# Performance work log

Hardware: AMD Instinct MI355X
Metric: run time of the kernel (lower is better)

## Reference

```python
import jax, jax.numpy as jnp
import numpy as np

B, S, D, H = 2, 2048, 1024, 16
HD = D // H

def setup_inputs() -> dict:
    key = jax.random.key(0)
    ks = jax.random.split(key, 9)
    s = 1.0 / np.sqrt(D)
    return {
        "x": jax.random.normal(ks[0], (B, S, D), dtype=jnp.float32),
        "Wq": jax.random.uniform(ks[1], (D, D), jnp.float32, -s, s),
        "bq": jax.random.uniform(ks[2], (D,), jnp.float32, -s, s),
        "Wk": jax.random.uniform(ks[3], (D, D), jnp.float32, -s, s),
        "bk": jax.random.uniform(ks[4], (D,), jnp.float32, -s, s),
        "Wv": jax.random.uniform(ks[5], (D, D), jnp.float32, -s, s),
        "bv": jax.random.uniform(ks[6], (D,), jnp.float32, -s, s),
        "Wo": jax.random.uniform(ks[7], (D, D), jnp.float32, -s, s),
        "bo": jax.random.uniform(ks[8], (D,), jnp.float32, -s, s),
    }

def reference(x, Wq, bq, Wk, bk, Wv, bv, Wo, bo):
    # project and split heads: [B,S,D] -> [B,H,S,HD]
    def heads(t):
        return t.reshape(B, S, H, HD).transpose(0, 2, 1, 3)
    q = heads(x @ Wq.T + bq)
    k = heads(x @ Wk.T + bk)
    v = heads(x @ Wv.T + bv)
    scores = jnp.einsum('bhqd,bhkd->bhqk', q, k) / np.sqrt(HD).astype(np.float32)
    attention_weights = jax.nn.softmax(scores, axis=-1)  # [B,H,S,S]
    out = jnp.einsum('bhqk,bhkd->bhqd', attention_weights, v)
    out = out.transpose(0, 2, 1, 3).reshape(B, S, D)
    out = out @ Wo.T + bo
    return out, attention_weights
```

## Files before the change

kernel.cpp:

```cpp
#include <hip/hip_runtime.h>
#include <stdint.h>

#define BB 2
#define SS 2048
#define DD 1024
#define HH 16
#define HDD 64

typedef _Float16 f16x8 __attribute__((ext_vector_type(8)));
typedef _Float16 f16x4 __attribute__((ext_vector_type(4)));
typedef float f32x4 __attribute__((ext_vector_type(4)));

#define MFMA16(a,b,c) __builtin_amdgcn_mfma_f32_16x16x32_f16((a),(b),(c),0,0,0)

__device__ __forceinline__ _Float16 toh(float v) { return (_Float16)v; }

__device__ __forceinline__ void gll16(const void* g, void* l) {
  __builtin_amdgcn_global_load_lds(
      (const __attribute__((address_space(1))) unsigned int*)g,
      (__attribute__((address_space(3))) unsigned int*)l, 16, 0, 0);
}

__global__ __launch_bounds__(256) void k_convert(
    const float* __restrict__ x, const float* __restrict__ Wq, const float* __restrict__ Wk,
    const float* __restrict__ Wv, const float* __restrict__ Wo, _Float16* __restrict__ ws) {
  int i = blockIdx.x * 256 + threadIdx.x;
  const float4* src; _Float16* dst; int idx;
  if (i < 1048576) { src = (const float4*)x; dst = ws; idx = i; }
  else {
    int j = i - 1048576;
    int wsel = j >> 18;
    idx = j & 262143;
    src = (const float4*)(wsel == 0 ? Wq : wsel == 1 ? Wk : wsel == 2 ? Wv : Wo);
    dst = ws + 4194304 + (size_t)wsel * 1048576;
  }
  float4 f = src[idx];
  f16x4 o = { toh(f.x), toh(f.y), toh(f.z), toh(f.w) };
  *(f16x4*)(dst + (size_t)idx * 4) = o;
}

__device__ __forceinline__ void stage2(const _Float16* g, _Float16* lds, int t) {
#pragma unroll
  for (int i = 0; i < 2; ++i) {
    const _Float16* src = g + (size_t)(i * 64 + (t >> 2)) * 1024 + (t & 3) * 8;
    gll16(src, lds + i * 2048 + t * 8);
  }
}

__device__ __forceinline__ void gemm_core(const _Float16* __restrict__ A,
                                          const _Float16* __restrict__ W,
                                          int bm, int bn, _Float16* As, _Float16* Bs,
                                          f32x4 (&acc)[4][4]) {
  const int t = threadIdx.x;
  const int l = t & 63, w = t >> 6;
  const int wr = w >> 1, wc = w & 1, li = l & 15, lg = l >> 4;
  const _Float16* Abase = A + (size_t)bm * 128 * 1024;
  const _Float16* Wbase = W + (size_t)bn * 128 * 1024;

  stage2(Abase, As, t);
  stage2(Wbase, Bs, t);
  int cur = 0;
  for (int kt = 0; kt < 32; ++kt) {
    __syncthreads();
    if (kt < 31) {
      stage2(Abase + (kt + 1) * 32, As + (cur ^ 1) * 4096, t);
      stage2(Wbase + (kt + 1) * 32, Bs + (cur ^ 1) * 4096, t);
    }
    const _Float16* Ab = As + cur * 4096;
    const _Float16* Bb = Bs + cur * 4096;
    f16x8 af[4], bfr[4];
#pragma unroll
    for (int m = 0; m < 4; ++m)
      af[m] = *(const f16x8*)(Ab + (wr * 64 + m * 16 + li) * 32 + lg * 8);
#pragma unroll
    for (int n = 0; n < 4; ++n)
      bfr[n] = *(const f16x8*)(Bb + (wc * 64 + n * 16 + li) * 32 + lg * 8);
    __builtin_amdgcn_s_setprio(1);
#pragma unroll
    for (int m = 0; m < 4; ++m)
#pragma unroll
      for (int n = 0; n < 4; ++n)
        acc[m][n] = MFMA16(af[m], bfr[n], acc[m][n]);
    __builtin_amdgcn_s_setprio(0);
    cur ^= 1;
  }
}

__global__ __launch_bounds__(256) void k_gemm_qkv(
    const _Float16* __restrict__ xb, const _Float16* __restrict__ wqb,
    const _Float16* __restrict__ wkb, const _Float16* __restrict__ wvb,
    const float* __restrict__ bq, const float* __restrict__ bk, const float* __restrict__ bv,
    _Float16* __restrict__ Qw, _Float16* __restrict__ Kw, _Float16* __restrict__ Vtw) {
  int mode = blockIdx.z;
  const _Float16* W = mode == 0 ? wqb : mode == 1 ? wkb : wvb;
  const float* bias = mode == 0 ? bq : mode == 1 ? bk : bv;
  __shared__ _Float16 As[8192], Bs[8192];
  f32x4 acc[4][4] = {};
  gemm_core(xb, W, blockIdx.y, blockIdx.x, As, Bs, acc);

  int t = threadIdx.x, l = t & 63, w = t >> 6, wr = w >> 1, wc = w & 1, li = l & 15, lg = l >> 4;
  int rb = blockIdx.y * 128 + wr * 64, cb = blockIdx.x * 128 + wc * 64;
  float scale = (mode == 0) ? 0.125f * 1.4426950408889634f : 1.0f;
#pragma unroll
  for (int n = 0; n < 4; ++n) {
    int col = cb + n * 16 + li;
    float bsv = bias[col];
    int hh = col >> 6, hd = col & 63;
#pragma unroll
    for (int m = 0; m < 4; ++m)
#pragma unroll
      for (int r = 0; r < 4; ++r) {
        int row = rb + m * 16 + lg * 4 + r;
        int bb = row >> 11, ssi = row & 2047;
        float val = (acc[m][n][r] + bsv) * scale;
        if (mode == 0)
          Qw[((size_t)(bb * HH + hh) * SS + ssi) * HDD + hd] = toh(val);
        else if (mode == 1)
          Kw[((size_t)(bb * HH + hh) * SS + ssi) * HDD + hd] = toh(val);
        else
          Vtw[((size_t)(bb * HH + hh) * HDD + hd) * SS + ssi] = toh(val);
      }
  }
}

__global__ __launch_bounds__(256) void k_flash(
    const _Float16* __restrict__ Qw, const _Float16* __restrict__ Kw,
    const _Float16* __restrict__ Vtw, float* __restrict__ mlb, _Float16* __restrict__ attnb) {
  int qb = blockIdx.x;
  int h = blockIdx.y, b = blockIdx.z;
  int t = threadIdx.x, l = t & 63, w = t >> 6;
  int li = l & 15, lg = l >> 4;
  size_t bh = (size_t)(b * HH + h);
  const _Float16* Qh = Qw + bh * SS * HDD;
  const _Float16* Kh = Kw + bh * SS * HDD;
  const _Float16* Vh = Vtw + bh * HDD * SS;
  int qrow = qb * 128 + w * 32;

  __shared__ _Float16 Kbuf[2][4096];
  __shared__ _Float16 Vbuf[2][4096];
  __shared__ _Float16 Wl[4][32][72];

  f16x8 aq[2][2];
#pragma unroll
  for (int qh = 0; qh < 2; ++qh)
#pragma unroll
    for (int s = 0; s < 2; ++s)
      aq[qh][s] = *(const f16x8*)&Qh[(size_t)(qrow + qh * 16 + li) * HDD + s * 32 + lg * 8];

  const f32x4 fzero = {0.f, 0.f, 0.f, 0.f};
  f32x4 oacc[2][4] = {{fzero, fzero, fzero, fzero}, {fzero, fzero, fzero, fzero}};
  float lsum[2][4] = {{0.f, 0.f, 0.f, 0.f}, {0.f, 0.f, 0.f, 0.f}};

  auto STAGE = [&](int kt, int sel) {
    int kb = kt * 64;
#pragma unroll
    for (int c2 = 0; c2 < 2; ++c2) {
      int s = c2 * 256 + t;
      int row = s >> 3, cc = (s & 7) ^ (row & 7);
      gll16(Kh + (size_t)(kb + row) * HDD + cc * 8, (void*)&Kbuf[sel][s * 8]);
      gll16(Vh + (size_t)row * SS + kb + cc * 8, (void*)&Vbuf[sel][s * 8]);
    }
  };

  STAGE(0, 0);
  __syncthreads();
  int cur = 0;
  for (int kt = 0; kt < 32; ++kt) {
    if (kt < 31) STAGE(kt + 1, cur ^ 1);
    const _Float16* Kb = Kbuf[cur];
    f32x4 sf[4][2];
    __builtin_amdgcn_s_setprio(1);
#pragma unroll
    for (int f = 0; f < 4; ++f) {
      int row = f * 16 + li;
      f16x8 k0 = *(const f16x8*)(Kb + row * 64 + ((lg ^ (row & 7)) * 8));
      f16x8 k1 = *(const f16x8*)(Kb + row * 64 + (((lg + 4) ^ (row & 7)) * 8));
#pragma unroll
      for (int qh = 0; qh < 2; ++qh) {
        f32x4 a = MFMA16(aq[qh][0], k0, fzero);
        sf[f][qh] = MFMA16(aq[qh][1], k1, a);
      }
    }
    __builtin_amdgcn_s_setprio(0);
#pragma unroll
    for (int f = 0; f < 4; ++f)
#pragma unroll
      for (int qh = 0; qh < 2; ++qh)
#pragma unroll
        for (int r = 0; r < 4; ++r) {
          float p = exp2f(sf[f][qh][r]);
          lsum[qh][r] += p;
          Wl[w][qh * 16 + lg * 4 + r][f * 16 + li] = toh(p);
        }
    f16x8 pa[2][2];
#pragma unroll
    for (int qh = 0; qh < 2; ++qh)
#pragma unroll
      for (int ks = 0; ks < 2; ++ks)
        pa[qh][ks] = *(const f16x8*)&Wl[w][qh * 16 + li][ks * 32 + lg * 8];
    const _Float16* Vb = Vbuf[cur];
    __builtin_amdgcn_s_setprio(1);
#pragma unroll
    for (int n = 0; n < 4; ++n) {
      int row = n * 16 + li;
      f16x8 v0 = *(const f16x8*)(Vb + row * 64 + ((lg ^ (row & 7)) * 8));
      f16x8 v1 = *(const f16x8*)(Vb + row * 64 + (((lg + 4) ^ (row & 7)) * 8));
#pragma unroll
      for (int qh = 0; qh < 2; ++qh) {
        oacc[qh][n] = MFMA16(pa[qh][0], v0, oacc[qh][n]);
        oacc[qh][n] = MFMA16(pa[qh][1], v1, oacc[qh][n]);
      }
    }
    __builtin_amdgcn_s_setprio(0);
    __syncthreads();
    cur ^= 1;
  }

#pragma unroll
  for (int d = 1; d < 16; d <<= 1)
#pragma unroll
    for (int qh = 0; qh < 2; ++qh)
#pragma unroll
      for (int r = 0; r < 4; ++r) lsum[qh][r] += __shfl_xor(lsum[qh][r], d);
  float rinv[2][4];
#pragma unroll
  for (int qh = 0; qh < 2; ++qh)
#pragma unroll
    for (int r = 0; r < 4; ++r) rinv[qh][r] = 1.0f / lsum[qh][r];

#pragma unroll
  for (int qh = 0; qh < 2; ++qh)
#pragma unroll
    for (int n = 0; n < 4; ++n)
#pragma unroll
      for (int r = 0; r < 4; ++r) {
        int q = qrow + qh * 16 + lg * 4 + r;
        attnb[((size_t)b * SS + q) * DD + h * 64 + n * 16 + li] =
            toh(oacc[qh][n][r] * rinv[qh][r]);
      }
  if (li == 0) {
#pragma unroll
    for (int qh = 0; qh < 2; ++qh)
#pragma unroll
      for (int r = 0; r < 4; ++r) {
        int q = qrow + qh * 16 + lg * 4 + r;
        mlb[bh * SS + q] = rinv[qh][r];
      }
  }
}

__global__ __launch_bounds__(256) void k_wts(
    const _Float16* __restrict__ Qw, const _Float16* __restrict__ Kw,
    const float* __restrict__ mlb, float* __restrict__ wts) {
  int ktile = blockIdx.x, qtile = blockIdx.y;
  size_t bh = blockIdx.z;
  const _Float16* Qh = Qw + bh * SS * HDD;
  const _Float16* Kh = Kw + bh * SS * HDD;
  __shared__ _Float16 As[8192], Bs[8192];
  int t = threadIdx.x, l = t & 63, w = t >> 6, wr = w >> 1, wc = w & 1, li = l & 15, lg = l >> 4;

#pragma unroll
  for (int c4 = 0; c4 < 4; ++c4) {
    int s = c4 * 256 + t;
    int row = s >> 3, cc = (s & 7) ^ (row & 7);
    gll16(Qh + (size_t)(qtile * 128 + row) * HDD + cc * 8, (void*)&As[s * 8]);
    gll16(Kh + (size_t)(ktile * 128 + row) * HDD + cc * 8, (void*)&Bs[s * 8]);
  }
  __syncthreads();

  f32x4 acc[4][4] = {};
#pragma unroll
  for (int s = 0; s < 2; ++s) {
    f16x8 af[4], bf[4];
#pragma unroll
    for (int m = 0; m < 4; ++m) {
      int row = wr * 64 + m * 16 + li;
      af[m] = *(const f16x8*)(As + row * 64 + (((s * 4 + lg) ^ (row & 7)) * 8));
    }
#pragma unroll
    for (int n = 0; n < 4; ++n) {
      int row = wc * 64 + n * 16 + li;
      bf[n] = *(const f16x8*)(Bs + row * 64 + (((s * 4 + lg) ^ (row & 7)) * 8));
    }
    __builtin_amdgcn_s_setprio(1);
#pragma unroll
    for (int m = 0; m < 4; ++m)
#pragma unroll
      for (int n = 0; n < 4; ++n)
        acc[m][n] = MFMA16(af[m], bf[n], acc[m][n]);
    __builtin_amdgcn_s_setprio(0);
  }

  int rb = qtile * 128 + wr * 64, cb = ktile * 128 + wc * 64;
#pragma unroll
  for (int m = 0; m < 4; ++m)
#pragma unroll
    for (int r = 0; r < 4; ++r) {
      int qr = rb + m * 16 + lg * 4 + r;
      float ri = mlb[bh * SS + qr];
      float* wb = wts + ((bh * SS + qr) * (size_t)SS) + cb;
#pragma unroll
      for (int n = 0; n < 4; ++n)
        wb[n * 16 + li] = exp2f(acc[m][n][r]) * ri;
    }
}

__global__ __launch_bounds__(256) void k_gemm_o(
    const _Float16* __restrict__ attnb, const _Float16* __restrict__ wob,
    const float* __restrict__ bo, float* __restrict__ outp) {
  __shared__ _Float16 As[8192], Bs[8192];
  f32x4 acc[4][4] = {};
  gemm_core(attnb, wob, blockIdx.y, blockIdx.x, As, Bs, acc);

  int t = threadIdx.x, l = t & 63, w = t >> 6, wr = w >> 1, wc = w & 1, li = l & 15, lg = l >> 4;
  int rb = blockIdx.y * 128 + wr * 64, cb = blockIdx.x * 128 + wc * 64;
#pragma unroll
  for (int n = 0; n < 4; ++n) {
    int col = cb + n * 16 + li;
    float bsv = bo[col];
#pragma unroll
    for (int m = 0; m < 4; ++m)
#pragma unroll
      for (int r = 0; r < 4; ++r) {
        int row = rb + m * 16 + lg * 4 + r;
        outp[(size_t)row * DD + col] = acc[m][n][r] + bsv;
      }
  }
}

extern "C" void kernel_launch(void* const* d_in, const int* in_sizes, int n_in,
                              void* d_out, int out_size, void* d_ws, size_t ws_size,
                              hipStream_t stream) {
  const float* x  = (const float*)d_in[0];
  const float* Wq = (const float*)d_in[1];
  const float* bq = (const float*)d_in[2];
  const float* Wk = (const float*)d_in[3];
  const float* bk = (const float*)d_in[4];
  const float* Wv = (const float*)d_in[5];
  const float* bv = (const float*)d_in[6];
  const float* Wo = (const float*)d_in[7];
  const float* bo = (const float*)d_in[8];

  _Float16* ws   = (_Float16*)d_ws;
  _Float16* xb   = ws;
  _Float16* wqb  = ws + 4194304;
  _Float16* wkb  = ws + 5242880;
  _Float16* wvb  = ws + 6291456;
  _Float16* wob  = ws + 7340032;
  _Float16* Qw   = ws + 8388608;
  _Float16* Kw   = ws + 12582912;
  _Float16* Vtw  = ws + 16777216;
  _Float16* attnb= ws + 20971520;
  float* mlb = (float*)(ws + 4194304);

  float* outp = (float*)d_out;
  float* wts  = outp + 4194304;

  k_convert<<<dim3(8192), dim3(256), 0, stream>>>(x, Wq, Wk, Wv, Wo, ws);
  k_gemm_qkv<<<dim3(8, 32, 3), dim3(256), 0, stream>>>(xb, wqb, wkb, wvb, bq, bk, bv, Qw, Kw, Vtw);
  k_flash<<<dim3(16, 16, 2), dim3(256), 0, stream>>>(Qw, Kw, Vtw, mlb, attnb);
  k_wts<<<dim3(16, 16, 32), dim3(256), 0, stream>>>(Qw, Kw, mlb, wts);
  k_gemm_o<<<dim3(8, 32, 1), dim3(256), 0, stream>>>(attnb, wob, bo, outp);
}
```

Before: 275.3 us.

## Split attention keys across two blocks with a reduce kernel and swizzle grids by XCD

The flash kernel now processes half of the key range per block, doubling the grid to 1024 blocks. Each block writes unnormalized fp16 partial outputs and row sums, and a new reduce kernel combines them, normalizes, and produces the attention output and inverse sums. Both the flash and attention-weight kernels use a linear grid remapped so neighbouring tiles of the same head land on the same XCD, for better L2 reuse. The cost is an extra launch, extra partial-result traffic, and fp16 rounding of the partial sums. The partial buffer reuses the tail of the weights output as scratch before k_wts overwrites it.

Result: slower. 291.0 us (+5.7%).

```diff
diff --git a/kernel.cpp b/kernel.cpp
--- a/kernel.cpp
+++ b/kernel.cpp
@@ -123,18 +123,21 @@
   }
 }
 
-__global__ __launch_bounds__(256) void k_flash(
+__global__ __launch_bounds__(256) void k_flash2(
     const _Float16* __restrict__ Qw, const _Float16* __restrict__ Kw,
-    const _Float16* __restrict__ Vtw, float* __restrict__ mlb, _Float16* __restrict__ attnb) {
-  int qb = blockIdx.x;
-  int h = blockIdx.y, b = blockIdx.z;
+    const _Float16* __restrict__ Vtw, _Float16* __restrict__ opart,
+    float* __restrict__ lpart) {
+  int lin = blockIdx.x;
+  int swz = (lin & 7) * 128 + (lin >> 3);
+  int qb = swz & 15, ks = (swz >> 4) & 1, bhi = swz >> 5;
   int t = threadIdx.x, l = t & 63, w = t >> 6;
   int li = l & 15, lg = l >> 4;
-  size_t bh = (size_t)(b * HH + h);
+  size_t bh = (size_t)bhi;
   const _Float16* Qh = Qw + bh * SS * HDD;
-  const _Float16* Kh = Kw + bh * SS * HDD;
+  const _Float16* Khs = Kw + bh * SS * HDD + (size_t)(ks * 1024) * HDD;
   const _Float16* Vh = Vtw + bh * HDD * SS;
   int qrow = qb * 128 + w * 32;
+  int kofs = ks * 1024;
 
   __shared__ _Float16 Kbuf[2][4096];
   __shared__ _Float16 Vbuf[2][4096];
@@ -157,16 +160,16 @@
     for (int c2 = 0; c2 < 2; ++c2) {
       int s = c2 * 256 + t;
       int row = s >> 3, cc = (s & 7) ^ (row & 7);
-      gll16(Kh + (size_t)(kb + row) * HDD + cc * 8, (void*)&Kbuf[sel][s * 8]);
-      gll16(Vh + (size_t)row * SS + kb + cc * 8, (void*)&Vbuf[sel][s * 8]);
+      gll16(Khs + (size_t)(kb + row) * HDD + cc * 8, (void*)&Kbuf[sel][s * 8]);
+      gll16(Vh + (size_t)row * SS + kofs + kb + cc * 8, (void*)&Vbuf[sel][s * 8]);
     }
   };
 
   STAGE(0, 0);
   __syncthreads();
   int cur = 0;
-  for (int kt = 0; kt < 32; ++kt) {
-    if (kt < 31) STAGE(kt + 1, cur ^ 1);
+  for (int kt = 0; kt < 16; ++kt) {
+    if (kt < 15) STAGE(kt + 1, cur ^ 1);
     const _Float16* Kb = Kbuf[cur];
     f32x4 sf[4][2];
     __builtin_amdgcn_s_setprio(1);
@@ -196,8 +199,8 @@
 #pragma unroll
     for (int qh = 0; qh < 2; ++qh)
 #pragma unroll
-      for (int ks = 0; ks < 2; ++ks)
-        pa[qh][ks] = *(const f16x8*)&Wl[w][qh * 16 + li][ks * 32 + lg * 8];
+      for (int kss = 0; kss < 2; ++kss)
+        pa[qh][kss] = *(const f16x8*)&Wl[w][qh * 16 + li][kss * 32 + lg * 8];
     const _Float16* Vb = Vbuf[cur];
     __builtin_amdgcn_s_setprio(1);
 #pragma unroll
@@ -222,38 +225,54 @@
     for (int qh = 0; qh < 2; ++qh)
 #pragma unroll
       for (int r = 0; r < 4; ++r) lsum[qh][r] += __shfl_xor(lsum[qh][r], d);
-  float rinv[2][4];
+
 #pragma unroll
   for (int qh = 0; qh < 2; ++qh)
 #pragma unroll
-    for (int r = 0; r < 4; ++r) rinv[qh][r] = 1.0f / lsum[qh][r];
-
-#pragma unroll
-  for (int qh = 0; qh < 2; ++qh)
-#pragma unroll
     for (int n = 0; n < 4; ++n)
 #pragma unroll
       for (int r = 0; r < 4; ++r) {
-        int q = qrow + qh * 16 + lg * 4 + r;
-        attnb[((size_t)b * SS + q) * DD + h * 64 + n * 16 + li] =
-            toh(oacc[qh][n][r] * rinv[qh][r]);
+        size_t row = bh * SS + qrow + qh * 16 + lg * 4 + r;
+        opart[(row * 2 + ks) * 64 + n * 16 + li] = toh(oacc[qh][n][r]);
       }
   if (li == 0) {
 #pragma unroll
     for (int qh = 0; qh < 2; ++qh)
 #pragma unroll
       for (int r = 0; r < 4; ++r) {
-        int q = qrow + qh * 16 + lg * 4 + r;
-        mlb[bh * SS + q] = rinv[qh][r];
-      }
-  }
+        size_t row = bh * SS + qrow + qh * 16 + lg * 4 + r;
+        lpart[row * 2 + ks] = lsum[qh][r];
+      }
+  }
+}
+
+__global__ __launch_bounds__(256) void k_reduce(
+    const _Float16* __restrict__ opart, const float* __restrict__ lpart,
+    float* __restrict__ mlb, _Float16* __restrict__ attnb) {
+  int idx = blockIdx.x * 256 + threadIdx.x;
+  int row = idx >> 3;
+  int dblk = idx & 7;
+  float2 lp = *(const float2*)&lpart[row * 2];
+  float rinv = 1.0f / (lp.x + lp.y);
+  const _Float16* ob = opart + ((size_t)row * 2) * 64 + dblk * 8;
+  f16x8 p0 = *(const f16x8*)ob;
+  f16x8 p1 = *(const f16x8*)(ob + 64);
+  int bh = row >> 11, q = row & 2047;
+  int b = bh >> 4, h = bh & 15;
+  f16x8 o;
+#pragma unroll
+  for (int j = 0; j < 8; ++j) o[j] = toh(((float)p0[j] + (float)p1[j]) * rinv);
+  *(f16x8*)&attnb[((size_t)(b * SS + q)) * DD + h * 64 + dblk * 8] = o;
+  if (dblk == 0) mlb[row] = rinv;
 }
 
 __global__ __launch_bounds__(256) void k_wts(
     const _Float16* __restrict__ Qw, const _Float16* __restrict__ Kw,
     const float* __restrict__ mlb, float* __restrict__ wts) {
-  int ktile = blockIdx.x, qtile = blockIdx.y;
-  size_t bh = blockIdx.z;
+  int lin = blockIdx.x;
+  int swz = (lin & 7) * 1024 + (lin >> 3);
+  int ktile = swz & 15, qtile = (swz >> 4) & 15;
+  size_t bh = (size_t)(swz >> 8);
   const _Float16* Qh = Qw + bh * SS * HDD;
   const _Float16* Kh = Kw + bh * SS * HDD;
   __shared__ _Float16 As[8192], Bs[8192];
@@ -351,14 +370,17 @@
   _Float16* Kw   = ws + 12582912;
   _Float16* Vtw  = ws + 16777216;
   _Float16* attnb= ws + 20971520;
-  float* mlb = (float*)(ws + 4194304);
+  float* mlb   = (float*)(ws + 4194304);
+  float* lpart = (float*)(ws + 5242880);
 
   float* outp = (float*)d_out;
   float* wts  = outp + 4194304;
+  _Float16* opart = (_Float16*)(outp + 134217728);
 
   k_convert<<<dim3(8192), dim3(256), 0, stream>>>(x, Wq, Wk, Wv, Wo, ws);
   k_gemm_qkv<<<dim3(8, 32, 3), dim3(256), 0, stream>>>(xb, wqb, wkb, wvb, bq, bk, bv, Qw, Kw, Vtw);
-  k_flash<<<dim3(16, 16, 2), dim3(256), 0, stream>>>(Qw, Kw, Vtw, mlb, attnb);
-  k_wts<<<dim3(16, 16, 32), dim3(256), 0, stream>>>(Qw, Kw, mlb, wts);
+  k_flash2<<<dim3(1024), dim3(256), 0, stream>>>(Qw, Kw, Vtw, opart, lpart);
+  k_reduce<<<dim3(2048), dim3(256), 0, stream>>>(opart, lpart, mlb, attnb);
+  k_wts<<<dim3(8192), dim3(256), 0, stream>>>(Qw, Kw, mlb, wts);
   k_gemm_o<<<dim3(8, 32, 1), dim3(256), 0, stream>>>(attnb, wob, bo, outp);
 }
```
